# Kernel optimization log

Hardware: AMD Instinct MI355X
Metric: run time of the kernel (lower is better)

## Reference

```python
import jax, jax.numpy as jnp
import numpy as np

N = 100000      # num_nodes
E = 1600000     # num_edges
IN_DIM = 6
EDGE_DIM = 2
H = 5           # heads
C = 5           # out_channels per head (hidden_dim)
D = H * C       # 25, hidden width
L = 3           # num_layers
INV_SQRT_C = np.float32(1.0 / np.sqrt(C))


def setup_inputs() -> dict:
    key = jax.random.key(0)
    ks = jax.random.split(key, 18)
    s = 0.1
    inp = {
        "x": jax.random.normal(ks[0], (N, IN_DIM), dtype=jnp.float32),
        "edge_index": jax.random.randint(ks[1], (2, E), 0, N, dtype=jnp.int64),
        "edge_attr": jax.random.normal(ks[2], (E, EDGE_DIM), dtype=jnp.float32),
        # input projection
        "Wi": jax.random.normal(ks[3], (IN_DIM, D), dtype=jnp.float32) * s,
        "bi": jnp.zeros((D,), dtype=jnp.float32),
        # per-layer TransformerConv params, stacked over layers
        "Wq": jax.random.normal(ks[4], (L, D, D), dtype=jnp.float32) * s,
        "bq": jnp.zeros((L, D), dtype=jnp.float32),
        "Wk": jax.random.normal(ks[5], (L, D, D), dtype=jnp.float32) * s,
        "bk": jnp.zeros((L, D), dtype=jnp.float32),
        "Wv": jax.random.normal(ks[6], (L, D, D), dtype=jnp.float32) * s,
        "bv": jnp.zeros((L, D), dtype=jnp.float32),
        "We": jax.random.normal(ks[7], (L, EDGE_DIM, D), dtype=jnp.float32) * s,  # lin_edge, no bias
        "Wskip": jax.random.normal(ks[8], (L, D, D), dtype=jnp.float32) * s,
        "bskip": jnp.zeros((L, D), dtype=jnp.float32),
        # output head
        "Wo": jax.random.normal(ks[9], (D, 1), dtype=jnp.float32) * s,
        "bo": jnp.zeros((1,), dtype=jnp.float32),
    }
    return inp


def _forward(x, edge_index, edge_attr, Wi, bi, Wq, bq, Wk, bk, Wv, bv, We, Wskip, bskip, Wo, bo):
    src, dst = edge_index[0], edge_index[1]
    h = x @ Wi + bi  # [N, D]
    for l in range(L):
        q = (h @ Wq[l] + bq[l]).reshape(N, H, C)
        k = (h @ Wk[l] + bk[l]).reshape(N, H, C)
        v = (h @ Wv[l] + bv[l]).reshape(N, H, C)
        e = (edge_attr @ We[l]).reshape(E, H, C)  # per-edge projection
        k_j = k[src] + e                           # [E, H, C]
        alpha = jnp.einsum('ehc,ehc->eh', q[dst], k_j) * INV_SQRT_C  # [E, H]
        # scatter-softmax over destination neighborhoods (PyG softmax)
        amax = jax.ops.segment_max(alpha, dst, num_segments=N)       # [N, H]
        ex = jnp.exp(alpha - amax[dst])
        denom = jax.ops.segment_sum(ex, dst, num_segments=N)         # [N, H]
        alpha = ex / (denom[dst] + 1e-16)
        msg = (v[src] + e) * alpha[:, :, None]                       # [E, H, C]
        out = jax.ops.segment_sum(msg, dst, num_segments=N).reshape(N, D)
        h = out + h @ Wskip[l] + bskip[l]          # root_weight skip
    return jax.nn.sigmoid(h @ Wo + bo)             # [N, 1]


def reference(x, edge_index, edge_attr, Wi, bi, Wq, bq, Wk, bk, Wv, bv, We, Wskip, bskip, Wo, bo):
    return _forward(x, edge_index, edge_attr, Wi, bi, Wq, bq, Wk, bk, Wv, bv, We, Wskip, bskip, Wo, bo)
```

## Files before the change

kernel.cpp:

```cpp
#include <hip/hip_runtime.h>
#include <hip/hip_bf16.h>
#include <math.h>

#define NN 100000
#define NE 1600000
#define IN_DIM 6
#define EDGE_DIM 2
#define HH 5
#define CC 5
#define DD 25
#define DS 32
#define INV_SQRT_C 0.4472135954999579f
#define NBUK 200
#define BUKW 500
#define CAP 10000
#define KPB 800
#define CH (NE / KPB)
#define NPB 48
#define NBLK ((NN + NPB - 1) / NPB)


__device__ __forceinline__ unsigned int f2bf(float f) {
    unsigned int u = __float_as_uint(f);
    return (u + 0x7fffu + ((u >> 16) & 1u)) >> 16;
}
__device__ __forceinline__ float bflo(unsigned int u) { return __uint_as_float(u << 16); }
__device__ __forceinline__ float bfhi(unsigned int u) { return __uint_as_float(u & 0xffff0000u); }

__global__ __launch_bounds__(256) void k_part(const int* __restrict__ ei,
                                              const float* __restrict__ ea,
                                              int* __restrict__ cursor,
                                              uint2* __restrict__ slab) {
    __shared__ int sdst[CH];
    __shared__ int scnt[NBUK];
    __shared__ int sbase[NBUK];
    __shared__ int swp[NBUK];
    int base = blockIdx.x * CH;
    for (int i = threadIdx.x; i < NBUK; i += 256) scnt[i] = 0;
    __syncthreads();
    for (int i = threadIdx.x; i < CH; i += 256) {
        int dst = ei[NE + base + i];
        sdst[i] = dst;
        atomicAdd(&scnt[dst / BUKW], 1);
    }
    __syncthreads();
    for (int i = threadIdx.x; i < NBUK; i += 256) {
        sbase[i] = i * CAP + atomicAdd(&cursor[i], scnt[i]);
        swp[i] = 0;
    }
    __syncthreads();
    for (int i = threadIdx.x; i < CH; i += 256) {
        int dst = sdst[i];
        int b = dst / BUKW;
        int src = ei[base + i];
        float2 eav = ((const float2*)ea)[base + i];
        int p = sbase[b] + atomicAdd(&swp[b], 1);
        uint2 r;
        r.x = (unsigned)src | ((unsigned)(dst - b * BUKW) << 17);
        r.y = f2bf(eav.x) | (f2bf(eav.y) << 16);
        slab[p] = r;
    }
}

__global__ __launch_bounds__(512) void k_place(const int* __restrict__ cursor,
                                               const uint2* __restrict__ slab,
                                               int* __restrict__ rowptr,
                                               uint2* __restrict__ csr) {
    __shared__ int hist[BUKW];
    __shared__ int cur[BUKW];
    __shared__ int s[512];
    int b = blockIdx.x;
    int t = threadIdx.x;
    int node0 = b * BUKW;
    int begin = b * CAP;
    int cnt = cursor[b];
    s[t] = (t < NBUK && t < b) ? cursor[t] : 0;
    __syncthreads();
    for (int off = 256; off > 0; off >>= 1) {
        if (t < off) s[t] += s[t + off];
        __syncthreads();
    }
    int bOff = s[0];
    __syncthreads();
    for (int i = t; i < BUKW; i += 512) hist[i] = 0;
    __syncthreads();
    for (int i = t; i < cnt; i += 512) {
        uint2 r = slab[begin + i];
        atomicAdd(&hist[r.x >> 17], 1);
    }
    __syncthreads();
    int hv = (t < BUKW) ? hist[t] : 0;
    s[t] = hv;
    __syncthreads();
    for (int off = 1; off < 512; off <<= 1) {
        int u = (t >= off) ? s[t - off] : 0;
        __syncthreads();
        s[t] += u;
        __syncthreads();
    }
    if (t < BUKW) {
        int o = bOff + s[t] - hv;
        rowptr[node0 + t] = o;
        cur[t] = o;
    }
    if (b == NBUK - 1 && t == 0) rowptr[NN] = NE;
    __syncthreads();
    for (int i = t; i < cnt; i += 512) {
        uint2 r = slab[begin + i];
        int dl = (int)(r.x >> 17);
        int p = atomicAdd(&cur[dl], 1);
        uint2 o;
        o.x = r.x & 0x1FFFFu;
        o.y = r.y;
        csr[p] = o;
    }
}

__global__ void k_input_proj(const float* __restrict__ x, const float* __restrict__ Wi,
                             const float* __restrict__ bi, float* __restrict__ h) {
    __shared__ float sW[IN_DIM * DD];
    __shared__ float sb[DD];
    int t = threadIdx.x;
    if (t < IN_DIM * DD) sW[t] = Wi[t];
    if (t < DD) sb[t] = bi[t];
    __syncthreads();
    int tid = blockIdx.x * blockDim.x + t;
    int n = tid / DD, d = tid - n * DD;
    if (n >= NN) return;
    float acc = sb[d];
    const float* xr = x + n * IN_DIM;
#pragma unroll
    for (int i = 0; i < IN_DIM; i++) acc += xr[i] * sW[i * DD + d];
    h[n * DS + d] = acc;
}

__global__ void k_qkv_skip(const float* __restrict__ h,
                           const float* __restrict__ Wq, const float* __restrict__ bq,
                           const float* __restrict__ Wk, const float* __restrict__ bk,
                           const float* __restrict__ Wv, const float* __restrict__ bv,
                           const float* __restrict__ Ws, const float* __restrict__ bs,
                           __hip_bfloat16* __restrict__ q, __hip_bfloat16* __restrict__ kv,
                           float* __restrict__ hout) {
    __shared__ float sWq[DD * DD], sWk[DD * DD], sWv[DD * DD], sWs[DD * DD];
    __shared__ float sb[4 * DD];
    for (int i = threadIdx.x; i < DD * DD; i += blockDim.x) {
        sWq[i] = Wq[i]; sWk[i] = Wk[i]; sWv[i] = Wv[i]; sWs[i] = Ws[i];
    }
    if (threadIdx.x < DD) {
        sb[threadIdx.x]          = bq[threadIdx.x];
        sb[DD + threadIdx.x]     = bk[threadIdx.x];
        sb[2 * DD + threadIdx.x] = bv[threadIdx.x];
        sb[3 * DD + threadIdx.x] = bs[threadIdx.x];
    }
    __syncthreads();
    int tid = blockIdx.x * blockDim.x + threadIdx.x;
    int n = tid / DD, d = tid - n * DD;
    if (n >= NN) return;
    float aq = sb[d], ak = sb[DD + d], av = sb[2 * DD + d], asv = sb[3 * DD + d];
    const float* hr = h + (size_t)n * DS;
#pragma unroll
    for (int i = 0; i < DD; i++) {
        float hv = hr[i];
        aq  += hv * sWq[i * DD + d];
        ak  += hv * sWk[i * DD + d];
        av  += hv * sWv[i * DD + d];
        asv += hv * sWs[i * DD + d];
    }
    int h5 = d / 5, c5 = d - 5 * h5;
    q[(size_t)n * 40 + 8 * h5 + c5] = __float2bfloat16(aq * INV_SQRT_C);
    kv[(size_t)n * 50 + 10 * h5 + c5]     = __float2bfloat16(ak);
    kv[(size_t)n * 50 + 10 * h5 + 5 + c5] = __float2bfloat16(av);
    hout[(size_t)n * DS + d] = asv;
}

__global__ __launch_bounds__(256) void k_edge_fused(
    const int* __restrict__ rowptr, const uint2* __restrict__ csr,
    const float* __restrict__ We, const __hip_bfloat16* __restrict__ q,
    const __hip_bfloat16* __restrict__ kv, float* __restrict__ hout,
    int fuse_head, const float* __restrict__ Wo, const float* __restrict__ bo,
    float* __restrict__ out) {
    __shared__ float sWe[EDGE_DIM * DD];
    __shared__ float sWo[DD];
    __shared__ float sbo;
    if (threadIdx.x < EDGE_DIM * DD) sWe[threadIdx.x] = We[threadIdx.x];
    if (threadIdx.x < DD) sWo[threadIdx.x] = Wo[threadIdx.x];
    if (threadIdx.x == 0) sbo = bo[0];
    __syncthreads();
    int lane = threadIdx.x & 63;
    int wv   = threadIdx.x >> 6;
    int grp  = lane / 5;
    int h    = lane - grp * 5;
    int node = blockIdx.x * NPB + wv * 12 + grp;
    bool act = (grp < 12) && (node < NN);

    int beg = 0, end = 0;
    float qa0 = 0, qa1 = 0, qa2 = 0, qa3 = 0, qa4 = 0, qwx = 0, qwy = 0;
    if (act) {
        beg = rowptr[node];
        end = rowptr[node + 1];
        uint4 qc = *(const uint4*)(q + (size_t)node * 40 + 8 * h);
        qa0 = bflo(qc.x); qa1 = bfhi(qc.x); qa2 = bflo(qc.y); qa3 = bfhi(qc.y); qa4 = bflo(qc.z);
        const float* wx = &sWe[5 * h];
        const float* wy = &sWe[DD + 5 * h];
        qwx = qa0 * wx[0] + qa1 * wx[1] + qa2 * wx[2] + qa3 * wx[3] + qa4 * wx[4];
        qwy = qa0 * wy[0] + qa1 * wy[1] + qa2 * wy[2] + qa3 * wy[3] + qa4 * wy[4];
    }

    float l = 0.f, Sx = 0.f, Sy = 0.f;
    float a0 = 0.f, a1 = 0.f, a2 = 0.f, a3 = 0.f, a4 = 0.f;

    int p = beg;
    uint2 rec;
    rec.x = 0; rec.y = 0;
    if (p < end) rec = csr[p];
    while (p < end) {
        int pn = p + 1;
        uint2 nrec = rec;
        if (pn < end) nrec = csr[pn];
        const unsigned int* kb =
            (const unsigned int*)(kv + (size_t)rec.x * 50 + 10 * h);
        unsigned int u0 = kb[0], u1 = kb[1], u2 = kb[2], u3 = kb[3], u4 = kb[4];
        float eax = bflo(rec.y), eay = bfhi(rec.y);
        float k0 = bflo(u0), k1 = bfhi(u0), k2 = bflo(u1), k3 = bfhi(u1), k4 = bflo(u2);
        float v0 = bfhi(u2), v1 = bflo(u3), v2 = bfhi(u3), v3 = bflo(u4), v4 = bfhi(u4);
        float s = qa0 * k0 + qa1 * k1 + qa2 * k2 + qa3 * k3 + qa4 * k4
                + eax * qwx + eay * qwy;
        float cf = __expf(s);
        l  += cf;
        Sx += cf * eax;
        Sy += cf * eay;
        a0 += cf * v0; a1 += cf * v1; a2 += cf * v2; a3 += cf * v3; a4 += cf * v4;
        rec = nrec;
        p = pn;
    }

    float dot = 0.f;
    if (act) {
        float inv = 1.0f / (l + 1e-16f);
        const float* wx = &sWe[5 * h];
        const float* wy = &sWe[DD + 5 * h];
        float* ho = hout + (size_t)node * DS + 5 * h;
        float n0 = ho[0] + (a0 + Sx * wx[0] + Sy * wy[0]) * inv;
        float n1 = ho[1] + (a1 + Sx * wx[1] + Sy * wy[1]) * inv;
        float n2 = ho[2] + (a2 + Sx * wx[2] + Sy * wy[2]) * inv;
        float n3 = ho[3] + (a3 + Sx * wx[3] + Sy * wy[3]) * inv;
        float n4 = ho[4] + (a4 + Sx * wx[4] + Sy * wy[4]) * inv;
        ho[0] = n0; ho[1] = n1; ho[2] = n2; ho[3] = n3; ho[4] = n4;
        if (fuse_head) {
            const float* wo = &sWo[5 * h];
            dot = n0 * wo[0] + n1 * wo[1] + n2 * wo[2] + n3 * wo[3] + n4 * wo[4];
        }
    }
    if (fuse_head) {
        float dsum = dot;
#pragma unroll
        for (int k = 1; k < 5; k++) dsum += __shfl(dot, (grp * 5 + k) & 63, 64);
        if (act && h == 0) out[node] = 1.0f / (1.0f + __expf(-(dsum + sbo)));
    }
}

extern "C" void kernel_launch(void* const* d_in, const int* in_sizes, int n_in,
                              void* d_out, int out_size, void* d_ws, size_t ws_size,
                              hipStream_t stream) {
    const float* x     = (const float*)d_in[0];
    const int*   ei    = (const int*)d_in[1];
    const float* ea    = (const float*)d_in[2];
    const float* Wi    = (const float*)d_in[3];
    const float* bi    = (const float*)d_in[4];
    const float* Wq    = (const float*)d_in[5];
    const float* bq    = (const float*)d_in[6];
    const float* Wk    = (const float*)d_in[7];
    const float* bk    = (const float*)d_in[8];
    const float* Wv    = (const float*)d_in[9];
    const float* bv    = (const float*)d_in[10];
    const float* We    = (const float*)d_in[11];
    const float* Wskip = (const float*)d_in[12];
    const float* bskip = (const float*)d_in[13];
    const float* Wo    = (const float*)d_in[14];
    const float* bo    = (const float*)d_in[15];
    float* out = (float*)d_out;
    (void)in_sizes; (void)n_in; (void)out_size; (void)ws_size;

    char* wsb = (char*)d_ws;
    size_t off = 0;
    auto alloc = [&](size_t bytes) {
        void* p = wsb + off;
        off += (bytes + 127) & ~(size_t)127;
        return p;
    };
    uint2* slab   = (uint2*)alloc((size_t)NBUK * CAP * sizeof(uint2));
    uint2* csr    = (uint2*)alloc((size_t)NE * sizeof(uint2));
    __hip_bfloat16* kvrec = (__hip_bfloat16*)alloc((size_t)NN * 50 * 2);
    __hip_bfloat16* qrec  = (__hip_bfloat16*)alloc((size_t)NN * 40 * 2);
    float* hA     = (float*)alloc((size_t)NN * DS * sizeof(float));
    float* hB     = (float*)alloc((size_t)NN * DS * sizeof(float));
    int*   rowptr = (int*)alloc((size_t)(NN + 1) * sizeof(int));
    int*   cursor = (int*)alloc((size_t)NBUK * sizeof(int));

    dim3 blk(256);
    int gND = (NN * DD + 255) / 256;

    hipMemsetAsync(cursor, 0, (size_t)NBUK * sizeof(int), stream);
    k_part<<<KPB, blk, 0, stream>>>(ei, ea, cursor, slab);
    k_place<<<NBUK, dim3(512), 0, stream>>>(cursor, slab, rowptr, csr);

    k_input_proj<<<gND, blk, 0, stream>>>(x, Wi, bi, hA);

    float* hc = hA;
    float* hn = hB;
    for (int l = 0; l < 3; l++) {
        k_qkv_skip<<<gND, blk, 0, stream>>>(hc,
                                            Wq + (size_t)l * DD * DD, bq + (size_t)l * DD,
                                            Wk + (size_t)l * DD * DD, bk + (size_t)l * DD,
                                            Wv + (size_t)l * DD * DD, bv + (size_t)l * DD,
                                            Wskip + (size_t)l * DD * DD, bskip + (size_t)l * DD,
                                            qrec, kvrec, hn);
        k_edge_fused<<<NBLK, blk, 0, stream>>>(rowptr, csr,
                                               We + (size_t)l * EDGE_DIM * DD,
                                               qrec, kvrec, hn,
                                               (l == 2) ? 1 : 0, Wo, bo, out);
        float* t = hc; hc = hn; hn = t;
    }
}
```

Measured before the change: 381.5 us.

## Sort nodes by degree for edge kernel and pad KV records to 128 bytes

Adds a counting sort of nodes by in-degree (histogram, scan, place) and has the edge kernel process nodes through this permutation, so lanes in a wavefront walk neighbor lists of similar length and less time is lost to divergence. It also pads each node's K/V record to 64 bf16 values, 128 bytes, so that each gathered head slice is one 16-byte load plus one 4-byte load instead of five scalar loads. The cost is three extra small kernels, an indirection through perm, scattered node access order for q/hout, and more gather bytes per record.

```diff
diff --git a/kernel.cpp b/kernel.cpp
--- a/kernel.cpp
+++ b/kernel.cpp
@@ -116,6 +116,44 @@
     }
 }
 
+__global__ void k_deghist(const int* __restrict__ rowptr, int* __restrict__ dhist) {
+    __shared__ int lh[256];
+    int t = threadIdx.x;
+    lh[t] = 0;
+    __syncthreads();
+    int i = blockIdx.x * 256 + t;
+    if (i < NN) {
+        int d = rowptr[i + 1] - rowptr[i];
+        atomicAdd(&lh[d > 255 ? 255 : d], 1);
+    }
+    __syncthreads();
+    if (lh[t]) atomicAdd(&dhist[t], lh[t]);
+}
+
+__global__ void k_degscan(const int* __restrict__ dhist, int* __restrict__ bincur) {
+    __shared__ int s[256];
+    int t = threadIdx.x;
+    int v = dhist[t];
+    s[t] = v;
+    __syncthreads();
+    for (int off = 1; off < 256; off <<= 1) {
+        int u = (t >= off) ? s[t - off] : 0;
+        __syncthreads();
+        s[t] += u;
+        __syncthreads();
+    }
+    bincur[t] = s[t] - v;
+}
+
+__global__ void k_degplace(const int* __restrict__ rowptr, int* __restrict__ bincur,
+                           int* __restrict__ perm) {
+    int i = blockIdx.x * 256 + threadIdx.x;
+    if (i >= NN) return;
+    int d = rowptr[i + 1] - rowptr[i];
+    int p = atomicAdd(&bincur[d > 255 ? 255 : d], 1);
+    perm[p] = i;
+}
+
 __global__ void k_input_proj(const float* __restrict__ x, const float* __restrict__ Wi,
                              const float* __restrict__ bi, float* __restrict__ h) {
     __shared__ float sW[IN_DIM * DD];
@@ -168,13 +206,16 @@
     }
     int h5 = d / 5, c5 = d - 5 * h5;
     q[(size_t)n * 40 + 8 * h5 + c5] = __float2bfloat16(aq * INV_SQRT_C);
-    kv[(size_t)n * 50 + 10 * h5 + c5]     = __float2bfloat16(ak);
-    kv[(size_t)n * 50 + 10 * h5 + 5 + c5] = __float2bfloat16(av);
+    size_t rb = (size_t)n * 64;
+    kv[rb + 8 * h5 + c5] = __float2bfloat16(ak);
+    if (c5 < 3) kv[rb + 8 * h5 + 5 + c5] = __float2bfloat16(av);
+    else        kv[rb + 40 + 2 * h5 + (c5 - 3)] = __float2bfloat16(av);
     hout[(size_t)n * DS + d] = asv;
 }
 
 __global__ __launch_bounds__(256) void k_edge_fused(
     const int* __restrict__ rowptr, const uint2* __restrict__ csr,
+    const int* __restrict__ perm,
     const float* __restrict__ We, const __hip_bfloat16* __restrict__ q,
     const __hip_bfloat16* __restrict__ kv, float* __restrict__ hout,
     int fuse_head, const float* __restrict__ Wo, const float* __restrict__ bo,
@@ -190,12 +231,14 @@
     int wv   = threadIdx.x >> 6;
     int grp  = lane / 5;
     int h    = lane - grp * 5;
-    int node = blockIdx.x * NPB + wv * 12 + grp;
-    bool act = (grp < 12) && (node < NN);
+    int idx  = blockIdx.x * NPB + wv * 12 + grp;
+    bool act = (grp < 12) && (idx < NN);
+    int node = 0;
 
     int beg = 0, end = 0;
     float qa0 = 0, qa1 = 0, qa2 = 0, qa3 = 0, qa4 = 0, qwx = 0, qwy = 0;
     if (act) {
+        node = perm[idx];
         beg = rowptr[node];
         end = rowptr[node + 1];
         uint4 qc = *(const uint4*)(q + (size_t)node * 40 + 8 * h);
@@ -217,12 +260,12 @@
         int pn = p + 1;
         uint2 nrec = rec;
         if (pn < end) nrec = csr[pn];
-        const unsigned int* kb =
-            (const unsigned int*)(kv + (size_t)rec.x * 50 + 10 * h);
-        unsigned int u0 = kb[0], u1 = kb[1], u2 = kb[2], u3 = kb[3], u4 = kb[4];
+        const __hip_bfloat16* base = kv + ((size_t)rec.x << 6);
+        uint4 A = *(const uint4*)(base + 8 * h);
+        unsigned int B = *(const unsigned int*)(base + 40 + 2 * h);
         float eax = bflo(rec.y), eay = bfhi(rec.y);
-        float k0 = bflo(u0), k1 = bfhi(u0), k2 = bflo(u1), k3 = bfhi(u1), k4 = bflo(u2);
-        float v0 = bfhi(u2), v1 = bflo(u3), v2 = bfhi(u3), v3 = bflo(u4), v4 = bfhi(u4);
+        float k0 = bflo(A.x), k1 = bfhi(A.x), k2 = bflo(A.y), k3 = bfhi(A.y), k4 = bflo(A.z);
+        float v0 = bfhi(A.z), v1 = bflo(A.w), v2 = bfhi(A.w), v3 = bflo(B), v4 = bfhi(B);
         float s = qa0 * k0 + qa1 * k1 + qa2 * k2 + qa3 * k3 + qa4 * k4
                 + eax * qwx + eay * qwy;
         float cf = __expf(s);
@@ -290,19 +333,27 @@
     };
     uint2* slab   = (uint2*)alloc((size_t)NBUK * CAP * sizeof(uint2));
     uint2* csr    = (uint2*)alloc((size_t)NE * sizeof(uint2));
-    __hip_bfloat16* kvrec = (__hip_bfloat16*)alloc((size_t)NN * 50 * 2);
+    __hip_bfloat16* kvrec = (__hip_bfloat16*)alloc((size_t)NN * 64 * 2);
     __hip_bfloat16* qrec  = (__hip_bfloat16*)alloc((size_t)NN * 40 * 2);
     float* hA     = (float*)alloc((size_t)NN * DS * sizeof(float));
     float* hB     = (float*)alloc((size_t)NN * DS * sizeof(float));
     int*   rowptr = (int*)alloc((size_t)(NN + 1) * sizeof(int));
-    int*   cursor = (int*)alloc((size_t)NBUK * sizeof(int));
+    int*   zeroed = (int*)alloc((size_t)(NBUK + 256) * sizeof(int));
+    int*   cursor = zeroed;
+    int*   dhist  = zeroed + NBUK;
+    int*   bincur = (int*)alloc(256 * sizeof(int));
+    int*   perm   = (int*)alloc((size_t)NN * sizeof(int));
 
     dim3 blk(256);
+    int gN  = (NN + 255) / 256;
     int gND = (NN * DD + 255) / 256;
 
-    hipMemsetAsync(cursor, 0, (size_t)NBUK * sizeof(int), stream);
+    hipMemsetAsync(zeroed, 0, (size_t)(NBUK + 256) * sizeof(int), stream);
     k_part<<<KPB, blk, 0, stream>>>(ei, ea, cursor, slab);
     k_place<<<NBUK, dim3(512), 0, stream>>>(cursor, slab, rowptr, csr);
+    k_deghist<<<gN, blk, 0, stream>>>(rowptr, dhist);
+    k_degscan<<<1, blk, 0, stream>>>(dhist, bincur);
+    k_degplace<<<gN, blk, 0, stream>>>(rowptr, bincur, perm);
 
     k_input_proj<<<gND, blk, 0, stream>>>(x, Wi, bi, hA);
 
@@ -315,7 +366,7 @@
                                             Wv + (size_t)l * DD * DD, bv + (size_t)l * DD,
                                             Wskip + (size_t)l * DD * DD, bskip + (size_t)l * DD,
                                             qrec, kvrec, hn);
-        k_edge_fused<<<NBLK, blk, 0, stream>>>(rowptr, csr,
+        k_edge_fused<<<NBLK, blk, 0, stream>>>(rowptr, csr, perm,
                                                We + (size_t)l * EDGE_DIM * DD,
                                                qrec, kvrec, hn,
                                                (l == 2) ? 1 : 0, Wo, bo, out);
```

After: 635.3 us. 66.5% more time.
